# Optimization experiments

Hardware: AMD Instinct MI355X
Metric: run time of the kernel (lower is better)

The kernel has to match this reference:

```python
import jax, jax.numpy as jnp
import numpy as np

N_NODES = 100000
N_EDGES = 3200000
ALPHA = 0.9
N_LAYERS = 10


def setup_inputs() -> dict:
    key = jax.random.key(0)
    ks = jax.random.split(key, 6)
    x = jax.random.normal(ks[0], (N_NODES, 512), dtype=jnp.float32)
    W_in = jax.random.normal(ks[1], (256, 512), dtype=jnp.float32) * (1.0 / np.sqrt(512))
    b_in = jnp.zeros((256,), dtype=jnp.float32)
    W_out = jax.random.normal(ks[2], (64, 256), dtype=jnp.float32) * (1.0 / np.sqrt(256))
    b_out = jnp.zeros((64,), dtype=jnp.float32)
    edge_index = jax.random.randint(ks[3], (2, N_EDGES), 0, N_NODES, dtype=jnp.int64)
    # ~1/avg_degree scale keeps the iterated propagation numerically stable
    edge_weight = jax.random.uniform(ks[4], (N_EDGES,), dtype=jnp.float32) * (1.0 / 32.0)
    return {"x": x, "W_in": W_in, "b_in": b_in, "W_out": W_out,
            "b_out": b_out, "edge_index": edge_index, "edge_weight": edge_weight}


def _spmm(edge_index, edge_weight, z, n_nodes):
    # out[dst] += w * z[src]  (COO SpMM via gather + segment_sum)
    src, dst = edge_index[0], edge_index[1]
    msg = z[src] * edge_weight[:, None]            # [E, C]
    return jax.ops.segment_sum(msg, dst, num_segments=n_nodes)


def reference(x, W_in, b_in, W_out, b_out, edge_index, edge_weight):
    n_nodes = x.shape[0]
    h = jax.nn.relu(x @ W_in.T + b_in)             # linear_in -> (dropout: eval, identity) -> relu
    z = h @ W_out.T + b_out                        # linear_out: [N, n_classes]
    z0 = z
    for _ in range(N_LAYERS):
        # APPNP propagation: alpha-weighted adj propagation + residual blend with x_0
        z = ALPHA * _spmm(edge_index, edge_weight, z, n_nodes) + (1.0 - ALPHA) * z0
    return z
```

## Files before the change

kernel.cpp:

```cpp
#include <hip/hip_runtime.h>
#include <hip/hip_bf16.h>

typedef __attribute__((ext_vector_type(8))) short bf16x8;
typedef __attribute__((ext_vector_type(4))) float f32x4;

__device__ __forceinline__ short f2b(float f) {
    unsigned u = __builtin_bit_cast(unsigned, f);
    unsigned r = (u + 0x7fffu + ((u >> 16) & 1u)) >> 16;
    return (short)r;
}
__device__ __forceinline__ unsigned f2bu(float f) {
    unsigned u = __builtin_bit_cast(unsigned, f);
    return ((u + 0x7fffu + ((u >> 16) & 1u)) >> 16) & 0xffffu;
}
__device__ __forceinline__ float blo(unsigned u) {
    return __builtin_bit_cast(float, u << 16);
}
__device__ __forceinline__ float bhi(unsigned u) {
    return __builtin_bit_cast(float, u & 0xffff0000u);
}

__global__ __launch_bounds__(256) void wprep(
    const float* __restrict__ W_in, const float* __restrict__ W_out,
    unsigned short* __restrict__ Wi_f, unsigned short* __restrict__ Wo_f)
{
    int o = blockIdx.x * 256 + threadIdx.x;
    if (o < 131072) {
        int j = o & 7, lane = (o >> 3) & 63, t = (o >> 9) & 15, kk = o >> 13;
        int n = t * 16 + (lane & 15);
        int k = kk * 32 + ((lane >> 4) << 3) + j;
        Wi_f[o] = (unsigned short)f2bu(W_in[n * 512 + k]);
    } else if (o < 131072 + 16384) {
        int o2 = o - 131072;
        int j = o2 & 7, lane = (o2 >> 3) & 63, t = (o2 >> 9) & 3, kk2 = o2 >> 11;
        int n = t * 16 + (lane & 15);
        int k = kk2 * 32 + ((lane >> 4) << 3) + j;
        Wo_f[o2] = (unsigned short)f2bu(W_out[n * 256 + k]);
    }
}

__global__ __launch_bounds__(256) void mlp(
    const float* __restrict__ x, const unsigned short* __restrict__ Wi_f,
    const float* __restrict__ b_in, const unsigned short* __restrict__ Wo_f,
    const float* __restrict__ b_out, unsigned short* __restrict__ z0, int M)
{
    __shared__ __align__(16) char smem[33280];
    short* Bt0 = (short*)smem;
    short* Bt1 = (short*)(smem + 16384);
    short* Hs  = (short*)smem;

    const int tid  = threadIdx.x;
    const int lane = tid & 63;
    const int w    = tid >> 6;
    const int row0 = blockIdx.x * 64;
    const int c    = lane & 15;
    const int qk   = lane >> 4;

    const int growA = row0 + 16 * w + c;
    const float* xrow = x + (size_t)(growA < M ? growA : (M - 1)) * 512 + qk * 8;

    f32x4 acc[16];
#pragma unroll
    for (int t = 0; t < 16; ++t) { acc[t][0]=0.f; acc[t][1]=0.f; acc[t][2]=0.f; acc[t][3]=0.f; }

    float4 av0 = *(const float4*)(xrow);
    float4 av1 = *(const float4*)(xrow + 4);
#pragma unroll
    for (int i = 0; i < 4; ++i) {
        int t = w * 4 + i;
        const unsigned short* g = Wi_f + ((size_t)t * 64 + lane) * 8;
        __builtin_amdgcn_global_load_lds(
            (const __attribute__((address_space(1))) unsigned int*)g,
            (__attribute__((address_space(3))) unsigned int*)(Bt0 + t * 512),
            16, 0, 0);
    }
    __syncthreads();

    for (int kk = 0; kk < 16; ++kk) {
        short* Bc = (kk & 1) ? Bt1 : Bt0;
        short* Bn = (kk & 1) ? Bt0 : Bt1;
        float4 a0 = av0, a1 = av1;
        if (kk < 15) {
            const float* xn = xrow + (kk + 1) * 32;
            av0 = *(const float4*)(xn);
            av1 = *(const float4*)(xn + 4);
#pragma unroll
            for (int i = 0; i < 4; ++i) {
                int t = w * 4 + i;
                const unsigned short* g = Wi_f + (((size_t)(kk + 1) * 16 + t) * 64 + lane) * 8;
                __builtin_amdgcn_global_load_lds(
                    (const __attribute__((address_space(1))) unsigned int*)g,
                    (__attribute__((address_space(3))) unsigned int*)(Bn + t * 512),
                    16, 0, 0);
            }
        }
        bf16x8 a;
        a[0] = (short)f2bu(a0.x); a[1] = (short)f2bu(a0.y);
        a[2] = (short)f2bu(a0.z); a[3] = (short)f2bu(a0.w);
        a[4] = (short)f2bu(a1.x); a[5] = (short)f2bu(a1.y);
        a[6] = (short)f2bu(a1.z); a[7] = (short)f2bu(a1.w);
#pragma unroll
        for (int t = 0; t < 16; ++t) {
            bf16x8 b = *(const bf16x8*)(Bc + (t * 64 + lane) * 8);
            acc[t] = __builtin_amdgcn_mfma_f32_16x16x32_bf16(a, b, acc[t], 0, 0, 0);
        }
        __syncthreads();
    }

#pragma unroll
    for (int t = 0; t < 16; ++t) {
        int col = 16 * t + c;
        float bv = b_in[col];
        int qb = col >> 3, j = col & 7;
#pragma unroll
        for (int r = 0; r < 4; ++r) {
            int row = 16 * w + qk * 4 + r;
            float h = acc[t][r] + bv;
            h = h > 0.f ? h : 0.f;
            Hs[qb * 520 + row * 8 + j] = f2b(h);
        }
    }
    __syncthreads();
    f32x4 acc2[4];
#pragma unroll
    for (int t = 0; t < 4; ++t) { acc2[t][0]=0.f; acc2[t][1]=0.f; acc2[t][2]=0.f; acc2[t][3]=0.f; }
#pragma unroll
    for (int kk2 = 0; kk2 < 8; ++kk2) {
        bf16x8 a2 = *(const bf16x8*)(Hs + (kk2 * 4 + qk) * 520 + (16 * w + c) * 8);
#pragma unroll
        for (int t = 0; t < 4; ++t) {
            bf16x8 b2 = *(const bf16x8*)(Wo_f + (((size_t)kk2 * 4 + t) * 64 + lane) * 8);
            acc2[t] = __builtin_amdgcn_mfma_f32_16x16x32_bf16(a2, b2, acc2[t], 0, 0, 0);
        }
    }
#pragma unroll
    for (int t = 0; t < 4; ++t) {
        int col = 16 * t + c;
        float bv = b_out[col];
#pragma unroll
        for (int r = 0; r < 4; ++r) {
            int grow = row0 + 16 * w + qk * 4 + r;
            if (grow < M) z0[(size_t)grow * 64 + col] = (unsigned short)f2bu(acc2[t][r] + bv);
        }
    }
}

#define CSR_CH   16384
#define MAXBUK   256

__global__ __launch_bounds__(256) void coarse_hist(
    const int* __restrict__ dst, int* __restrict__ M, int E, int nbuk)
{
    __shared__ int cnt[MAXBUK];
    int tid = threadIdx.x, blk = blockIdx.x;
    for (int i = tid; i < nbuk; i += 256) cnt[i] = 0;
    __syncthreads();
    int e0 = blk * CSR_CH, e1 = e0 + CSR_CH; if (e1 > E) e1 = E;
    for (int e = e0 + tid; e < e1; e += 256) atomicAdd(&cnt[dst[e] >> 9], 1);
    __syncthreads();
    for (int i = tid; i < nbuk; i += 256) M[blk * nbuk + i] = cnt[i];
}

__global__ __launch_bounds__(256) void bucket_scan(
    int* __restrict__ M, int* __restrict__ bucketBase, int nblk, int nbuk)
{
    __shared__ int tot[MAXBUK];
    int tid = threadIdx.x;
    for (int r = tid; r < nbuk; r += 256) {
        int s = 0;
        for (int k = 0; k < nblk; ++k) s += M[k * nbuk + r];
        tot[r] = s;
    }
    __syncthreads();
    if (tid == 0) {
        int s = 0;
        for (int r = 0; r < nbuk; ++r) { int t = tot[r]; tot[r] = s; bucketBase[r] = s; s += t; }
        bucketBase[nbuk] = s;
    }
    __syncthreads();
    for (int r = tid; r < nbuk; r += 256) {
        int s = tot[r];
        for (int k = 0; k < nblk; ++k) { int t = M[k * nbuk + r]; M[k * nbuk + r] = s; s += t; }
    }
}

__global__ __launch_bounds__(256) void coarse_scatter(
    const int* __restrict__ src, const int* __restrict__ dst,
    const float* __restrict__ ew, const int* __restrict__ M,
    int4* __restrict__ tmp, int E, int nbuk)
{
    __shared__ int off[MAXBUK];
    int tid = threadIdx.x, blk = blockIdx.x;
    for (int i = tid; i < nbuk; i += 256) off[i] = M[blk * nbuk + i];
    __syncthreads();
    int e0 = blk * CSR_CH, e1 = e0 + CSR_CH; if (e1 > E) e1 = E;
    for (int e = e0 + tid; e < e1; e += 256) {
        int d = dst[e];
        int pos = atomicAdd(&off[d >> 9], 1);
        tmp[pos] = make_int4(src[e], __builtin_bit_cast(int, ew[e]), d, 0);
    }
}

__global__ __launch_bounds__(256) void fine_sort(
    const int4* __restrict__ tmp, const int* __restrict__ bucketBase,
    int2* __restrict__ csr, int* __restrict__ rowptr, int N, int E)
{
    __shared__ int fc[512];
    __shared__ int fo[512];
    __shared__ int wsum[5];
    int b = blockIdx.x, tid = threadIdx.x;
    int base = bucketBase[b], cnt = bucketBase[b + 1] - base;
    int node0 = b << 9;

    fc[tid] = 0; fc[tid + 256] = 0;
    __syncthreads();
    for (int i = tid; i < cnt; i += 256)
        atomicAdd(&fc[tmp[base + i].z - node0], 1);
    __syncthreads();

    int lane = tid & 63, wid = tid >> 6;
    int runbase = 0;
    for (int h = 0; h < 2; ++h) {
        int v = fc[h * 256 + tid];
        int x = v;
#pragma unroll
        for (int off = 1; off < 64; off <<= 1) { int y = __shfl_up(x, off); if (lane >= off) x += y; }
        if (lane == 63) wsum[wid] = x;
        __syncthreads();
        if (tid == 0) { int s = 0; for (int k = 0; k < 4; ++k) { int t = wsum[k]; wsum[k] = s; s += t; } wsum[4] = s; }
        __syncthreads();
        fo[h * 256 + tid] = runbase + wsum[wid] + x - v;
        runbase += wsum[4];
        __syncthreads();
    }

    for (int i = tid; i < 512; i += 256) {
        int node = node0 + i;
        if (node < N) rowptr[node] = base + fo[i];
    }
    if (b == 0 && tid == 0) rowptr[N] = E;
    __syncthreads();

    for (int i = tid; i < cnt; i += 256) {
        int4 ed = tmp[base + i];
        int pos = atomicAdd(&fo[ed.z - node0], 1);
        csr[base + pos] = make_int2(ed.x, ed.y);
    }
}

__global__ __launch_bounds__(256) void prop_kernel(
    const int* __restrict__ rowptr, const int2* __restrict__ csr,
    const unsigned short* __restrict__ zin, const unsigned short* __restrict__ z0,
    unsigned short* __restrict__ zout_b, float* __restrict__ zout_f,
    int n, int final_layer)
{
    int lane = threadIdx.x & 63;
    int node = blockIdx.x * 4 + (threadIdx.x >> 6);
    if (node >= n) return;
    int beg = rowptr[node], end = rowptr[node + 1];
    const int sub = lane >> 3;
    const int k8  = lane & 7;

    float acc[8];
#pragma unroll
    for (int i = 0; i < 8; ++i) acc[i] = 0.f;

    for (int b = beg; b < end; b += 64) {
        int e = b + lane;
        int2 ed = (e < end) ? csr[e] : make_int2(0, 0);
        int cnt = end - b; if (cnt > 64) cnt = 64;
        int groups = (cnt + 7) >> 3;
        for (int j = 0; j < groups; ++j) {
            int idx = j * 8 + sub;
            int sj = __shfl(ed.x, idx);
            int wb = __shfl(ed.y, idx);
            if (idx < cnt) {
                float wj = __builtin_bit_cast(float, wb);
                uint4 v = *(const uint4*)(zin + (size_t)sj * 64 + k8 * 8);
                acc[0] += wj * blo(v.x); acc[1] += wj * bhi(v.x);
                acc[2] += wj * blo(v.y); acc[3] += wj * bhi(v.y);
                acc[4] += wj * blo(v.z); acc[5] += wj * bhi(v.z);
                acc[6] += wj * blo(v.w); acc[7] += wj * bhi(v.w);
            }
        }
    }
#pragma unroll
    for (int off = 8; off < 64; off <<= 1) {
#pragma unroll
        for (int i = 0; i < 8; ++i) acc[i] += __shfl_xor(acc[i], off);
    }
    if (sub == 0) {
        uint4 zv = *(const uint4*)(z0 + (size_t)node * 64 + k8 * 8);
        float o0 = 0.9f * acc[0] + 0.1f * blo(zv.x);
        float o1 = 0.9f * acc[1] + 0.1f * bhi(zv.x);
        float o2 = 0.9f * acc[2] + 0.1f * blo(zv.y);
        float o3 = 0.9f * acc[3] + 0.1f * bhi(zv.y);
        float o4 = 0.9f * acc[4] + 0.1f * blo(zv.z);
        float o5 = 0.9f * acc[5] + 0.1f * bhi(zv.z);
        float o6 = 0.9f * acc[6] + 0.1f * blo(zv.w);
        float o7 = 0.9f * acc[7] + 0.1f * bhi(zv.w);
        if (final_layer) {
            float* dp = zout_f + (size_t)node * 64 + k8 * 8;
            *(float4*)dp       = make_float4(o0, o1, o2, o3);
            *(float4*)(dp + 4) = make_float4(o4, o5, o6, o7);
        } else {
            uint4 pv;
            pv.x = f2bu(o0) | (f2bu(o1) << 16);
            pv.y = f2bu(o2) | (f2bu(o3) << 16);
            pv.z = f2bu(o4) | (f2bu(o5) << 16);
            pv.w = f2bu(o6) | (f2bu(o7) << 16);
            *(uint4*)(zout_b + (size_t)node * 64 + k8 * 8) = pv;
        }
    }
}

static inline size_t align_up(size_t v, size_t a) { return (v + a - 1) & ~(a - 1); }

extern "C" void kernel_launch(void* const* d_in, const int* in_sizes, int n_in,
                              void* d_out, int out_size, void* d_ws, size_t ws_size,
                              hipStream_t stream)
{
    const float* x     = (const float*)d_in[0];
    const float* W_in  = (const float*)d_in[1];
    const float* b_in  = (const float*)d_in[2];
    const float* W_out = (const float*)d_in[3];
    const float* b_out = (const float*)d_in[4];
    const int*   ei    = (const int*)d_in[5];
    const float* ew    = (const float*)d_in[6];

    const int N = in_sizes[0] / 512;
    const int E = in_sizes[6];
    const int* e_src = ei;
    const int* e_dst = ei + E;

    const int nbuk = (N + 511) >> 9;
    const int nblk = (E + CSR_CH - 1) / CSR_CH;

    char* p = (char*)d_ws;
    size_t zbytes = align_up((size_t)N * 64 * sizeof(unsigned short), 256);
    unsigned short* z0b = (unsigned short*)p; p += zbytes;
    unsigned short* Wi_f = (unsigned short*)p; p += align_up(131072 * 2, 256);
    unsigned short* Wo_f = (unsigned short*)p; p += align_up(16384 * 2, 256);
    int2* csr   = (int2*)p; p += align_up((size_t)E * 8, 256);
    int* rowptr = (int*)p;  p += align_up((size_t)(N + 1) * 4, 256);
    int* M      = (int*)p;  p += align_up((size_t)nblk * nbuk * 4, 256);
    int* bucketBase = (int*)p; p += align_up((size_t)(nbuk + 1) * 4, 256);
    int4* tmp   = (int4*)p; p += align_up((size_t)E * 16, 256);
    unsigned short* zA = (unsigned short*)tmp;
    unsigned short* zB = zA + (size_t)N * 64;

    wprep<<<(131072 + 16384 + 255) / 256, 256, 0, stream>>>(W_in, W_out, Wi_f, Wo_f);
    mlp<<<(N + 63) / 64, 256, 0, stream>>>(x, Wi_f, b_in, Wo_f, b_out, z0b, N);

    coarse_hist<<<nblk, 256, 0, stream>>>(e_dst, M, E, nbuk);
    bucket_scan<<<1, 256, 0, stream>>>(M, bucketBase, nblk, nbuk);
    coarse_scatter<<<nblk, 256, 0, stream>>>(e_src, e_dst, ew, M, tmp, E, nbuk);
    fine_sort<<<nbuk, 256, 0, stream>>>(tmp, bucketBase, csr, rowptr, N, E);

    float* out_f = (float*)d_out;
    int pgrid = (N + 3) / 4;
    for (int i = 0; i < 10; ++i) {
        const unsigned short* zin = (i == 0) ? z0b : ((i & 1) ? zA : zB);
        unsigned short* zoutb = (i & 1) ? zB : zA;
        prop_kernel<<<pgrid, 256, 0, stream>>>(rowptr, csr, zin, z0b,
                                               zoutb, out_f, N, (i == 9) ? 1 : 0);
    }
}
```

Measured before the change: 1.157 ms.

## Partition SpMM edges into four source-node stripes for cache locality

Edges are bucketed by (source stripe, destination block), so each propagation layer becomes four passes. Each pass gathers only from a quarter of the node features, a working set meant to fit in L2/LLC and cut DRAM traffic from the random gathers. Partial sums go to an fp32 accumulator buffer in global memory. This adds four times the kernel launches and rowptr reads, plus extra fp32 read/write traffic per node per stripe. Edge-list and accumulator accesses use nontemporal loads and stores so they do not evict the gathered features.

```diff
diff --git a/kernel.cpp b/kernel.cpp
--- a/kernel.cpp
+++ b/kernel.cpp
@@ -3,6 +3,7 @@
 
 typedef __attribute__((ext_vector_type(8))) short bf16x8;
 typedef __attribute__((ext_vector_type(4))) float f32x4;
+typedef __attribute__((ext_vector_type(4))) unsigned int u32x4;
 
 __device__ __forceinline__ short f2b(float f) {
     unsigned u = __builtin_bit_cast(unsigned, f);
@@ -147,72 +148,80 @@
 
 #define CSR_CH   16384
 #define MAXBUK   256
+#define FB       2048
 
 __global__ __launch_bounds__(256) void coarse_hist(
-    const int* __restrict__ dst, int* __restrict__ M, int E, int nbuk)
+    const int* __restrict__ src, const int* __restrict__ dst,
+    int* __restrict__ M, int E, int nbuk2, int nb1, int qs)
 {
     __shared__ int cnt[MAXBUK];
     int tid = threadIdx.x, blk = blockIdx.x;
-    for (int i = tid; i < nbuk; i += 256) cnt[i] = 0;
+    for (int i = tid; i < nbuk2; i += 256) cnt[i] = 0;
     __syncthreads();
     int e0 = blk * CSR_CH, e1 = e0 + CSR_CH; if (e1 > E) e1 = E;
-    for (int e = e0 + tid; e < e1; e += 256) atomicAdd(&cnt[dst[e] >> 9], 1);
-    __syncthreads();
-    for (int i = tid; i < nbuk; i += 256) M[blk * nbuk + i] = cnt[i];
+    for (int e = e0 + tid; e < e1; e += 256) {
+        int key = (src[e] / qs) * nb1 + (dst[e] >> 11);
+        atomicAdd(&cnt[key], 1);
+    }
+    __syncthreads();
+    for (int i = tid; i < nbuk2; i += 256) M[blk * nbuk2 + i] = cnt[i];
 }
 
 __global__ __launch_bounds__(256) void bucket_scan(
-    int* __restrict__ M, int* __restrict__ bucketBase, int nblk, int nbuk)
+    int* __restrict__ M, int* __restrict__ bucketBase, int nblk, int nbuk2)
 {
     __shared__ int tot[MAXBUK];
     int tid = threadIdx.x;
-    for (int r = tid; r < nbuk; r += 256) {
+    for (int r = tid; r < nbuk2; r += 256) {
         int s = 0;
-        for (int k = 0; k < nblk; ++k) s += M[k * nbuk + r];
+        for (int k = 0; k < nblk; ++k) s += M[k * nbuk2 + r];
         tot[r] = s;
     }
     __syncthreads();
     if (tid == 0) {
         int s = 0;
-        for (int r = 0; r < nbuk; ++r) { int t = tot[r]; tot[r] = s; bucketBase[r] = s; s += t; }
-        bucketBase[nbuk] = s;
-    }
-    __syncthreads();
-    for (int r = tid; r < nbuk; r += 256) {
+        for (int r = 0; r < nbuk2; ++r) { int t = tot[r]; tot[r] = s; bucketBase[r] = s; s += t; }
+        bucketBase[nbuk2] = s;
+    }
+    __syncthreads();
+    for (int r = tid; r < nbuk2; r += 256) {
         int s = tot[r];
-        for (int k = 0; k < nblk; ++k) { int t = M[k * nbuk + r]; M[k * nbuk + r] = s; s += t; }
+        for (int k = 0; k < nblk; ++k) { int t = M[k * nbuk2 + r]; M[k * nbuk2 + r] = s; s += t; }
     }
 }
 
 __global__ __launch_bounds__(256) void coarse_scatter(
     const int* __restrict__ src, const int* __restrict__ dst,
     const float* __restrict__ ew, const int* __restrict__ M,
-    int4* __restrict__ tmp, int E, int nbuk)
+    int4* __restrict__ tmp, int E, int nbuk2, int nb1, int qs)
 {
     __shared__ int off[MAXBUK];
     int tid = threadIdx.x, blk = blockIdx.x;
-    for (int i = tid; i < nbuk; i += 256) off[i] = M[blk * nbuk + i];
+    for (int i = tid; i < nbuk2; i += 256) off[i] = M[blk * nbuk2 + i];
     __syncthreads();
     int e0 = blk * CSR_CH, e1 = e0 + CSR_CH; if (e1 > E) e1 = E;
     for (int e = e0 + tid; e < e1; e += 256) {
-        int d = dst[e];
-        int pos = atomicAdd(&off[d >> 9], 1);
-        tmp[pos] = make_int4(src[e], __builtin_bit_cast(int, ew[e]), d, 0);
+        int s = src[e], d = dst[e];
+        int key = (s / qs) * nb1 + (d >> 11);
+        int pos = atomicAdd(&off[key], 1);
+        tmp[pos] = make_int4(s, __builtin_bit_cast(int, ew[e]), d, 0);
     }
 }
 
 __global__ __launch_bounds__(256) void fine_sort(
     const int4* __restrict__ tmp, const int* __restrict__ bucketBase,
-    int2* __restrict__ csr, int* __restrict__ rowptr, int N, int E)
-{
-    __shared__ int fc[512];
-    __shared__ int fo[512];
+    int2* __restrict__ csr, int* __restrict__ rowptr4,
+    int N, int E, int nb1)
+{
+    __shared__ int fc[FB];
+    __shared__ int fo[FB];
     __shared__ int wsum[5];
     int b = blockIdx.x, tid = threadIdx.x;
     int base = bucketBase[b], cnt = bucketBase[b + 1] - base;
-    int node0 = b << 9;
-
-    fc[tid] = 0; fc[tid + 256] = 0;
+    int stripe = b / nb1;
+    int node0  = (b % nb1) << 11;
+
+    for (int i = tid; i < FB; i += 256) fc[i] = 0;
     __syncthreads();
     for (int i = tid; i < cnt; i += 256)
         atomicAdd(&fc[tmp[base + i].z - node0], 1);
@@ -220,7 +229,7 @@
 
     int lane = tid & 63, wid = tid >> 6;
     int runbase = 0;
-    for (int h = 0; h < 2; ++h) {
+    for (int h = 0; h < FB / 256; ++h) {
         int v = fc[h * 256 + tid];
         int x = v;
 #pragma unroll
@@ -234,11 +243,11 @@
         __syncthreads();
     }
 
-    for (int i = tid; i < 512; i += 256) {
+    for (int i = tid; i < FB; i += 256) {
         int node = node0 + i;
-        if (node < N) rowptr[node] = base + fo[i];
-    }
-    if (b == 0 && tid == 0) rowptr[N] = E;
+        if (node < N) rowptr4[(size_t)stripe * N + node] = base + fo[i];
+    }
+    if (b == 0 && tid == 0) rowptr4[(size_t)4 * N] = E;
     __syncthreads();
 
     for (int i = tid; i < cnt; i += 256) {
@@ -248,16 +257,17 @@
     }
 }
 
-__global__ __launch_bounds__(256) void prop_kernel(
-    const int* __restrict__ rowptr, const int2* __restrict__ csr,
+__global__ __launch_bounds__(256) void prop_stripe(
+    const int* __restrict__ rowptr4, const int2* __restrict__ csr,
     const unsigned short* __restrict__ zin, const unsigned short* __restrict__ z0,
-    unsigned short* __restrict__ zout_b, float* __restrict__ zout_f,
-    int n, int final_layer)
+    float* __restrict__ zacc, unsigned short* __restrict__ zout_b,
+    float* __restrict__ zout_f, int n, int s, int final_layer)
 {
     int lane = threadIdx.x & 63;
     int node = blockIdx.x * 4 + (threadIdx.x >> 6);
     if (node >= n) return;
-    int beg = rowptr[node], end = rowptr[node + 1];
+    const int* rp = rowptr4 + (size_t)s * n;
+    int beg = rp[node], end = rp[node + 1];
     const int sub = lane >> 3;
     const int k8  = lane & 7;
 
@@ -265,15 +275,18 @@
 #pragma unroll
     for (int i = 0; i < 8; ++i) acc[i] = 0.f;
 
+    const long long* cp = (const long long*)csr;
     for (int b = beg; b < end; b += 64) {
         int e = b + lane;
-        int2 ed = (e < end) ? csr[e] : make_int2(0, 0);
+        long long edp = (e < end) ? __builtin_nontemporal_load(cp + e) : 0ll;
+        int edx = (int)edp;
+        int edy = (int)(edp >> 32);
         int cnt = end - b; if (cnt > 64) cnt = 64;
         int groups = (cnt + 7) >> 3;
         for (int j = 0; j < groups; ++j) {
             int idx = j * 8 + sub;
-            int sj = __shfl(ed.x, idx);
-            int wb = __shfl(ed.y, idx);
+            int sj = __shfl(edx, idx);
+            int wb = __shfl(edy, idx);
             if (idx < cnt) {
                 float wj = __builtin_bit_cast(float, wb);
                 uint4 v = *(const uint4*)(zin + (size_t)sj * 64 + k8 * 8);
@@ -290,26 +303,51 @@
         for (int i = 0; i < 8; ++i) acc[i] += __shfl_xor(acc[i], off);
     }
     if (sub == 0) {
-        uint4 zv = *(const uint4*)(z0 + (size_t)node * 64 + k8 * 8);
-        float o0 = 0.9f * acc[0] + 0.1f * blo(zv.x);
-        float o1 = 0.9f * acc[1] + 0.1f * bhi(zv.x);
-        float o2 = 0.9f * acc[2] + 0.1f * blo(zv.y);
-        float o3 = 0.9f * acc[3] + 0.1f * bhi(zv.y);
-        float o4 = 0.9f * acc[4] + 0.1f * blo(zv.z);
-        float o5 = 0.9f * acc[5] + 0.1f * bhi(zv.z);
-        float o6 = 0.9f * acc[6] + 0.1f * blo(zv.w);
-        float o7 = 0.9f * acc[7] + 0.1f * bhi(zv.w);
-        if (final_layer) {
-            float* dp = zout_f + (size_t)node * 64 + k8 * 8;
-            *(float4*)dp       = make_float4(o0, o1, o2, o3);
-            *(float4*)(dp + 4) = make_float4(o4, o5, o6, o7);
+        float* zp = zacc + (size_t)node * 64 + k8 * 8;
+        if (s == 0) {
+            u32x4 zv = __builtin_nontemporal_load(
+                (const u32x4*)(z0 + (size_t)node * 64 + k8 * 8));
+            f32x4 lo, hi;
+            lo[0] = 0.9f * acc[0] + 0.1f * blo(zv.x);
+            lo[1] = 0.9f * acc[1] + 0.1f * bhi(zv.x);
+            lo[2] = 0.9f * acc[2] + 0.1f * blo(zv.y);
+            lo[3] = 0.9f * acc[3] + 0.1f * bhi(zv.y);
+            hi[0] = 0.9f * acc[4] + 0.1f * blo(zv.z);
+            hi[1] = 0.9f * acc[5] + 0.1f * bhi(zv.z);
+            hi[2] = 0.9f * acc[6] + 0.1f * blo(zv.w);
+            hi[3] = 0.9f * acc[7] + 0.1f * bhi(zv.w);
+            __builtin_nontemporal_store(lo, (f32x4*)zp);
+            __builtin_nontemporal_store(hi, (f32x4*)(zp + 4));
         } else {
-            uint4 pv;
-            pv.x = f2bu(o0) | (f2bu(o1) << 16);
-            pv.y = f2bu(o2) | (f2bu(o3) << 16);
-            pv.z = f2bu(o4) | (f2bu(o5) << 16);
-            pv.w = f2bu(o6) | (f2bu(o7) << 16);
-            *(uint4*)(zout_b + (size_t)node * 64 + k8 * 8) = pv;
+            f32x4 p0 = __builtin_nontemporal_load((const f32x4*)zp);
+            f32x4 p1 = __builtin_nontemporal_load((const f32x4*)(zp + 4));
+            float o0 = p0[0] + 0.9f * acc[0];
+            float o1 = p0[1] + 0.9f * acc[1];
+            float o2 = p0[2] + 0.9f * acc[2];
+            float o3 = p0[3] + 0.9f * acc[3];
+            float o4 = p1[0] + 0.9f * acc[4];
+            float o5 = p1[1] + 0.9f * acc[5];
+            float o6 = p1[2] + 0.9f * acc[6];
+            float o7 = p1[3] + 0.9f * acc[7];
+            if (s < 3) {
+                f32x4 lo, hi;
+                lo[0]=o0; lo[1]=o1; lo[2]=o2; lo[3]=o3;
+                hi[0]=o4; hi[1]=o5; hi[2]=o6; hi[3]=o7;
+                __builtin_nontemporal_store(lo, (f32x4*)zp);
+                __builtin_nontemporal_store(hi, (f32x4*)(zp + 4));
+            } else if (final_layer) {
+                float* dp = zout_f + (size_t)node * 64 + k8 * 8;
+                *(float4*)dp       = make_float4(o0, o1, o2, o3);
+                *(float4*)(dp + 4) = make_float4(o4, o5, o6, o7);
+            } else {
+                u32x4 pv;
+                pv.x = f2bu(o0) | (f2bu(o1) << 16);
+                pv.y = f2bu(o2) | (f2bu(o3) << 16);
+                pv.z = f2bu(o4) | (f2bu(o5) << 16);
+                pv.w = f2bu(o6) | (f2bu(o7) << 16);
+                __builtin_nontemporal_store(
+                    pv, (u32x4*)(zout_b + (size_t)node * 64 + k8 * 8));
+            }
         }
     }
 }
@@ -333,36 +371,42 @@
     const int* e_src = ei;
     const int* e_dst = ei + E;
 
-    const int nbuk = (N + 511) >> 9;
-    const int nblk = (E + CSR_CH - 1) / CSR_CH;
+    const int qs    = (N + 3) / 4;
+    const int nb1   = (N + FB - 1) / FB;
+    const int nbuk2 = 4 * nb1;
+    const int nblk  = (E + CSR_CH - 1) / CSR_CH;
 
     char* p = (char*)d_ws;
     size_t zbytes = align_up((size_t)N * 64 * sizeof(unsigned short), 256);
     unsigned short* z0b = (unsigned short*)p; p += zbytes;
     unsigned short* Wi_f = (unsigned short*)p; p += align_up(131072 * 2, 256);
     unsigned short* Wo_f = (unsigned short*)p; p += align_up(16384 * 2, 256);
-    int2* csr   = (int2*)p; p += align_up((size_t)E * 8, 256);
-    int* rowptr = (int*)p;  p += align_up((size_t)(N + 1) * 4, 256);
-    int* M      = (int*)p;  p += align_up((size_t)nblk * nbuk * 4, 256);
-    int* bucketBase = (int*)p; p += align_up((size_t)(nbuk + 1) * 4, 256);
-    int4* tmp   = (int4*)p; p += align_up((size_t)E * 16, 256);
-    unsigned short* zA = (unsigned short*)tmp;
-    unsigned short* zB = zA + (size_t)N * 64;
+    int2* csr    = (int2*)p; p += align_up((size_t)E * 8, 256);
+    int* rowptr4 = (int*)p;  p += align_up(((size_t)4 * N + 1) * 4, 256);
+    int* M       = (int*)p;  p += align_up((size_t)nblk * nbuk2 * 4, 256);
+    int* bucketBase = (int*)p; p += align_up((size_t)(nbuk2 + 1) * 4, 256);
+    int4* tmp    = (int4*)p; p += align_up((size_t)E * 16, 256);
+    unsigned short* zA   = (unsigned short*)tmp;
+    unsigned short* zB   = zA + (size_t)N * 64;
+    float*          zacc = (float*)(zB + (size_t)N * 64);
 
     wprep<<<(131072 + 16384 + 255) / 256, 256, 0, stream>>>(W_in, W_out, Wi_f, Wo_f);
     mlp<<<(N + 63) / 64, 256, 0, stream>>>(x, Wi_f, b_in, Wo_f, b_out, z0b, N);
 
-    coarse_hist<<<nblk, 256, 0, stream>>>(e_dst, M, E, nbuk);
-    bucket_scan<<<1, 256, 0, stream>>>(M, bucketBase, nblk, nbuk);
-    coarse_scatter<<<nblk, 256, 0, stream>>>(e_src, e_dst, ew, M, tmp, E, nbuk);
-    fine_sort<<<nbuk, 256, 0, stream>>>(tmp, bucketBase, csr, rowptr, N, E);
+    coarse_hist<<<nblk, 256, 0, stream>>>(e_src, e_dst, M, E, nbuk2, nb1, qs);
+    bucket_scan<<<1, 256, 0, stream>>>(M, bucketBase, nblk, nbuk2);
+    coarse_scatter<<<nblk, 256, 0, stream>>>(e_src, e_dst, ew, M, tmp, E, nbuk2, nb1, qs);
+    fine_sort<<<nbuk2, 256, 0, stream>>>(tmp, bucketBase, csr, rowptr4, N, E, nb1);
 
     float* out_f = (float*)d_out;
     int pgrid = (N + 3) / 4;
     for (int i = 0; i < 10; ++i) {
         const unsigned short* zin = (i == 0) ? z0b : ((i & 1) ? zA : zB);
         unsigned short* zoutb = (i & 1) ? zB : zA;
-        prop_kernel<<<pgrid, 256, 0, stream>>>(rowptr, csr, zin, z0b,
-                                               zoutb, out_f, N, (i == 9) ? 1 : 0);
-    }
-}
+        for (int s = 0; s < 4; ++s) {
+            prop_stripe<<<pgrid, 256, 0, stream>>>(rowptr4, csr, zin, z0b,
+                                                   zacc, zoutb, out_f, N, s,
+                                                   (i == 9) ? 1 : 0);
+        }
+    }
+}
```

New measurement: 2.338 ms. +102.0%, slower.
